# Optimization experiments

Hardware: AMD Instinct MI355X
Metric: run time of the kernel (lower is better)

Reference implementation:

```python
import jax, jax.numpy as jnp
import numpy as np

B, S, D = 4, 4096, 256


def setup_inputs() -> dict:
    key = jax.random.key(0)
    ks = jax.random.split(key, 8)
    inv = 1.0 / np.sqrt(D)
    return {
        "input_tensor": jax.random.normal(ks[0], (B, S, D), dtype=jnp.float32),
        "attention_mask": jax.random.randint(ks[1], (B, S, S), 0, 2) == 1,
        "Wq": jax.random.uniform(ks[2], (D, D), jnp.float32, -inv, inv),
        "bq": jax.random.uniform(ks[3], (D,), jnp.float32, -inv, inv),
        "Wk": jax.random.uniform(ks[4], (D, D), jnp.float32, -inv, inv),
        "bk": jax.random.uniform(ks[5], (D,), jnp.float32, -inv, inv),
        "Wv": jax.random.uniform(ks[6], (D, D), jnp.float32, -inv, inv),
        "bv": jax.random.uniform(ks[7], (D,), jnp.float32, -inv, inv),
    }


def reference(input_tensor, attention_mask, Wq, bq, Wk, bk, Wv, bv):
    # Linear projections: y = x @ W.T + b  (nn.Linear convention, W is [out,in])
    query = jnp.einsum("bsd,ed->bse", input_tensor, Wq) + bq
    key = jnp.einsum("bsd,ed->bse", input_tensor, Wk) + bk
    value = jnp.einsum("bsd,ed->bse", input_tensor, Wv) + bv
    # Faithful quirk: original scales by sqrt(query.size(1)) == sqrt(seq_len)
    scale = jnp.asarray(query.shape[1], query.dtype) ** 0.5
    scores = jnp.einsum("bqd,bkd->bqk", query, key) / scale  # [B,S,S]
    scores = jnp.where(attention_mask, jnp.asarray(-1e9, scores.dtype), scores)
    attn = jax.nn.softmax(scores, axis=-1)
    # dropout with p=0.0 is identity (eval-mode reference)
    context = jnp.einsum("bqk,bkd->bqd", attn, value)
    return context
```

## Files before the change

### kernel.cpp

```cpp
#include <hip/hip_runtime.h>
#include <hip/hip_bf16.h>
#include <stdint.h>

#define BB 4
#define SS 4096
#define DD 256

typedef __attribute__((ext_vector_type(4))) float f32x4;
typedef __attribute__((ext_vector_type(8))) short s16x8;

__device__ __forceinline__ ushort f2bf(float f) {
  __hip_bfloat16 h = __float2bfloat16(f);
  return __builtin_bit_cast(ushort, h);
}

__global__ void convert_kernel(const float* __restrict__ X,
                               const float* __restrict__ Wq,
                               const float* __restrict__ Wk,
                               const float* __restrict__ Wv,
                               const float* __restrict__ bq,
                               const float* __restrict__ bk,
                               const float* __restrict__ bv,
                               ushort* __restrict__ Xb,
                               ushort* __restrict__ Wb,
                               float* __restrict__ bias) {
  int tid = blockIdx.x * blockDim.x + threadIdx.x;
  int stride = gridDim.x * blockDim.x;
  const int NX4 = (BB * SS * DD) / 4;
  for (int i = tid; i < NX4; i += stride) {
    float4 v = ((const float4*)X)[i];
    ushort4 o = { f2bf(v.x), f2bf(v.y), f2bf(v.z), f2bf(v.w) };
    ((ushort4*)Xb)[i] = o;
  }
  const int NW4 = (DD * DD) / 4;
  for (int i = tid; i < NW4; i += stride) {
    float4 a = ((const float4*)Wq)[i];
    float4 b = ((const float4*)Wk)[i];
    float4 c = ((const float4*)Wv)[i];
    ushort4 oa = { f2bf(a.x), f2bf(a.y), f2bf(a.z), f2bf(a.w) };
    ushort4 ob = { f2bf(b.x), f2bf(b.y), f2bf(b.z), f2bf(b.w) };
    ushort4 oc = { f2bf(c.x), f2bf(c.y), f2bf(c.z), f2bf(c.w) };
    ((ushort4*)Wb)[i]           = oa;
    ((ushort4*)Wb)[NW4 + i]     = ob;
    ((ushort4*)Wb)[2 * NW4 + i] = oc;
  }
  if (tid < DD) {
    bias[tid]          = bq[tid];
    bias[DD + tid]     = bk[tid];
    bias[2 * DD + tid] = bv[tid];
  }
}

#define LROW 40

__global__ __launch_bounds__(256) void proj_gemm(const ushort* __restrict__ Xb,
                                                 const ushort* __restrict__ Wb,
                                                 const float* __restrict__ bias,
                                                 ushort* __restrict__ Qb,
                                                 ushort* __restrict__ Kb,
                                                 ushort* __restrict__ Vt) {
  __shared__ ushort Al[128 * LROW];
  __shared__ ushort Bl[128 * LROW];
  const int m0 = blockIdx.x * 128;
  const int n0 = blockIdx.y * 128;
  const int t = threadIdx.x;
  const int lane = t & 63;
  const int w = t >> 6;
  const int wr = w & 1, wc = w >> 1;
  const int col = lane & 15;
  const int quad = lane >> 4;

  f32x4 acc[4][4];
#pragma unroll
  for (int i = 0; i < 4; i++)
#pragma unroll
    for (int j = 0; j < 4; j++) acc[i][j] = f32x4{0.f, 0.f, 0.f, 0.f};

  const int ci0 = t, ci1 = 256 + t;
  const int r0 = ci0 >> 2, c0 = ci0 & 3;
  const int r1 = ci1 >> 2, c1 = ci1 & 3;

  s16x8 pa0 = *(const s16x8*)(Xb + (m0 + r0) * DD + c0 * 8);
  s16x8 pa1 = *(const s16x8*)(Xb + (m0 + r1) * DD + c1 * 8);
  s16x8 pb0 = *(const s16x8*)(Wb + (n0 + r0) * DD + c0 * 8);
  s16x8 pb1 = *(const s16x8*)(Wb + (n0 + r1) * DD + c1 * 8);

  for (int kk = 0; kk < DD; kk += 32) {
    __syncthreads();
    *(s16x8*)&Al[r0 * LROW + c0 * 8] = pa0;
    *(s16x8*)&Al[r1 * LROW + c1 * 8] = pa1;
    *(s16x8*)&Bl[r0 * LROW + c0 * 8] = pb0;
    *(s16x8*)&Bl[r1 * LROW + c1 * 8] = pb1;
    __syncthreads();
    const int kn = kk + 32;
    if (kn < DD) {
      pa0 = *(const s16x8*)(Xb + (m0 + r0) * DD + kn + c0 * 8);
      pa1 = *(const s16x8*)(Xb + (m0 + r1) * DD + kn + c1 * 8);
      pb0 = *(const s16x8*)(Wb + (n0 + r0) * DD + kn + c0 * 8);
      pb1 = *(const s16x8*)(Wb + (n0 + r1) * DD + kn + c1 * 8);
    }
    s16x8 af[4], bfr[4];
#pragma unroll
    for (int mi = 0; mi < 4; mi++)
      af[mi] = *(const s16x8*)&Al[(wr * 64 + mi * 16 + col) * LROW + quad * 8];
#pragma unroll
    for (int ni = 0; ni < 4; ni++)
      bfr[ni] = *(const s16x8*)&Bl[(wc * 64 + ni * 16 + col) * LROW + quad * 8];
#pragma unroll
    for (int mi = 0; mi < 4; mi++)
#pragma unroll
      for (int ni = 0; ni < 4; ni++)
        acc[mi][ni] = __builtin_amdgcn_mfma_f32_16x16x32_bf16(af[mi], bfr[ni], acc[mi][ni], 0, 0, 0);
  }

  const int region = n0 >> 8;
#pragma unroll
  for (int mi = 0; mi < 4; mi++) {
    const int gm = m0 + wr * 64 + mi * 16 + quad * 4;
#pragma unroll
    for (int ni = 0; ni < 4; ni++) {
      const int gn = n0 + wc * 64 + ni * 16 + col;
      const float bb = bias[gn];
      f32x4 v = acc[mi][ni];
      if (region == 0) {
#pragma unroll
        for (int rg = 0; rg < 4; rg++)
          Qb[(gm + rg) * DD + gn] = f2bf((v[rg] + bb) * 0.015625f);
      } else if (region == 1) {
        const int d = gn - 256;
#pragma unroll
        for (int rg = 0; rg < 4; rg++)
          Kb[(gm + rg) * DD + d] = f2bf(v[rg] + bb);
      } else {
        const int d = gn - 512;
        const int b = gm >> 12;
        const int s = gm & (SS - 1);
        ushort4 o = { f2bf(v[0] + bb), f2bf(v[1] + bb), f2bf(v[2] + bb), f2bf(v[3] + bb) };
        *(ushort4*)&Vt[((size_t)(b << 8) + d) * SS + s] = o;
      }
    }
  }
}

#define NKT 32
#define KROW 264
#define VROW 40
#define PROW 40

__global__ __launch_bounds__(256) void attn_kernel(const ushort* __restrict__ Qb,
                                                   const ushort* __restrict__ Kb,
                                                   const ushort* __restrict__ Vt,
                                                   const int* __restrict__ mask,
                                                   float* __restrict__ out) {
  __shared__ ushort Kl[NKT * KROW];
  __shared__ ushort Vl[DD * VROW];
  __shared__ ushort Pl[4][16 * PROW];

  const int qt = blockIdx.x;
  const int b = blockIdx.y;
  const int t = threadIdx.x;
  const int lane = t & 63;
  const int w = t >> 6;
  const int col = lane & 15;
  const int quad = lane >> 4;

  const int q0 = qt * 64;
  const int qrow = q0 + w * 16;

  s16x8 qf[8];
  {
    const ushort* qp = Qb + ((size_t)b * SS + qrow + col) * DD + quad * 8;
#pragma unroll
    for (int dc = 0; dc < 8; dc++) qf[dc] = *(const s16x8*)(qp + dc * 32);
  }

  int kr[4], kc[4], vd[4], vc[4];
#pragma unroll
  for (int i = 0; i < 4; i++) {
    const int ci = i * 256 + t;
    kr[i] = ci >> 5; kc[i] = ci & 31;
    vd[i] = ci >> 2; vc[i] = ci & 3;
  }

  const ushort* Kg = Kb + (size_t)b * SS * DD;
  const ushort* Vg = Vt + (size_t)b * DD * SS;
  const int* Mg = mask + ((size_t)b * SS + q0 + w * 16 + quad * 4) * SS;

  f32x4 Oc[16];
#pragma unroll
  for (int i = 0; i < 16; i++) Oc[i] = f32x4{0.f, 0.f, 0.f, 0.f};
  float m_i[4] = {-INFINITY, -INFINITY, -INFINITY, -INFINITY};
  float l_i[4] = {0.f, 0.f, 0.f, 0.f};

  s16x8 pk[4], pv[4];
  int pm[2][4];
#pragma unroll
  for (int i = 0; i < 4; i++) {
    pk[i] = *(const s16x8*)(Kg + (size_t)kr[i] * DD + kc[i] * 8);
    pv[i] = *(const s16x8*)(Vg + (size_t)vd[i] * SS + vc[i] * 8);
  }
#pragma unroll
  for (int jt = 0; jt < 2; jt++)
#pragma unroll
    for (int rg = 0; rg < 4; rg++) pm[jt][rg] = Mg[rg * SS + jt * 16 + col];

  const int NT = SS / NKT;
  for (int tt = 0; tt < NT; tt++) {
    __syncthreads();
#pragma unroll
    for (int i = 0; i < 4; i++) {
      *(s16x8*)&Kl[kr[i] * KROW + kc[i] * 8] = pk[i];
      *(s16x8*)&Vl[vd[i] * VROW + vc[i] * 8] = pv[i];
    }
    __syncthreads();
    int mcur[2][4];
#pragma unroll
    for (int jt = 0; jt < 2; jt++)
#pragma unroll
      for (int rg = 0; rg < 4; rg++) mcur[jt][rg] = pm[jt][rg];
    if (tt + 1 < NT) {
      const int k0n = (tt + 1) * NKT;
#pragma unroll
      for (int i = 0; i < 4; i++) {
        pk[i] = *(const s16x8*)(Kg + ((size_t)k0n + kr[i]) * DD + kc[i] * 8);
        pv[i] = *(const s16x8*)(Vg + (size_t)vd[i] * SS + k0n + vc[i] * 8);
      }
#pragma unroll
      for (int jt = 0; jt < 2; jt++)
#pragma unroll
        for (int rg = 0; rg < 4; rg++) pm[jt][rg] = Mg[rg * SS + k0n + jt * 16 + col];
    }

    f32x4 st[2];
#pragma unroll
    for (int jt = 0; jt < 2; jt++) {
      f32x4 s = f32x4{0.f, 0.f, 0.f, 0.f};
#pragma unroll
      for (int dc = 0; dc < 8; dc++) {
        s16x8 kb = *(const s16x8*)&Kl[(jt * 16 + col) * KROW + dc * 32 + quad * 8];
        s = __builtin_amdgcn_mfma_f32_16x16x32_bf16(qf[dc], kb, s, 0, 0, 0);
      }
      st[jt] = s;
    }
#pragma unroll
    for (int jt = 0; jt < 2; jt++)
#pragma unroll
      for (int rg = 0; rg < 4; rg++)
        if (mcur[jt][rg]) st[jt][rg] = -1e9f;

    float al[4];
#pragma unroll
    for (int rg = 0; rg < 4; rg++) {
      float v = fmaxf(st[0][rg], st[1][rg]);
      v = fmaxf(v, __shfl_xor(v, 1));
      v = fmaxf(v, __shfl_xor(v, 2));
      v = fmaxf(v, __shfl_xor(v, 4));
      v = fmaxf(v, __shfl_xor(v, 8));
      const float mn = fmaxf(m_i[rg], v);
      al[rg] = __expf(m_i[rg] - mn);
      m_i[rg] = mn;
    }
#pragma unroll
    for (int rg = 0; rg < 4; rg++) {
      const float p0 = __expf(st[0][rg] - m_i[rg]);
      const float p1 = __expf(st[1][rg] - m_i[rg]);
      st[0][rg] = p0; st[1][rg] = p1;
      float s2 = p0 + p1;
      s2 += __shfl_xor(s2, 1);
      s2 += __shfl_xor(s2, 2);
      s2 += __shfl_xor(s2, 4);
      s2 += __shfl_xor(s2, 8);
      l_i[rg] = l_i[rg] * al[rg] + s2;
    }
#pragma unroll
    for (int dt = 0; dt < 16; dt++)
#pragma unroll
      for (int rg = 0; rg < 4; rg++) Oc[dt][rg] *= al[rg];

#pragma unroll
    for (int jt = 0; jt < 2; jt++)
#pragma unroll
      for (int rg = 0; rg < 4; rg++)
        Pl[w][(quad * 4 + rg) * PROW + jt * 16 + col] = f2bf(st[jt][rg]);
    s16x8 pa = *(const s16x8*)&Pl[w][col * PROW + quad * 8];

#pragma unroll
    for (int dt = 0; dt < 16; dt++) {
      s16x8 vb = *(const s16x8*)&Vl[(dt * 16 + col) * VROW + quad * 8];
      Oc[dt] = __builtin_amdgcn_mfma_f32_16x16x32_bf16(pa, vb, Oc[dt], 0, 0, 0);
    }
  }

  float inv[4];
#pragma unroll
  for (int rg = 0; rg < 4; rg++) inv[rg] = 1.0f / l_i[rg];
  float* op = out + ((size_t)b * SS + qrow + quad * 4) * DD;
#pragma unroll
  for (int dt = 0; dt < 16; dt++)
#pragma unroll
    for (int rg = 0; rg < 4; rg++)
      op[rg * DD + dt * 16 + col] = Oc[dt][rg] * inv[rg];
}

extern "C" void kernel_launch(void* const* d_in, const int* in_sizes, int n_in,
                              void* d_out, int out_size, void* d_ws, size_t ws_size,
                              hipStream_t stream) {
  const float* X  = (const float*)d_in[0];
  const int* mask = (const int*)d_in[1];
  const float* Wq = (const float*)d_in[2];
  const float* bq = (const float*)d_in[3];
  const float* Wk = (const float*)d_in[4];
  const float* bk = (const float*)d_in[5];
  const float* Wv = (const float*)d_in[6];
  const float* bv = (const float*)d_in[7];
  float* out = (float*)d_out;

  ushort* base = (ushort*)d_ws;
  ushort* Xb = base;
  ushort* Wb = Xb + (size_t)BB * SS * DD;
  ushort* Qb = Wb + (size_t)3 * DD * DD;
  ushort* Kb = Qb + (size_t)BB * SS * DD;
  ushort* Vt = Kb + (size_t)BB * SS * DD;
  float* bias = (float*)(Vt + (size_t)BB * SS * DD);

  convert_kernel<<<1024, 256, 0, stream>>>(X, Wq, Wk, Wv, bq, bk, bv, Xb, Wb, bias);
  proj_gemm<<<dim3(128, 6), 256, 0, stream>>>(Xb, Wb, bias, Qb, Kb, Vt);
  attn_kernel<<<dim3(64, 4), 256, 0, stream>>>(Qb, Kb, Vt, mask, out);
}
```

Baseline: 619.4 us.

## Split attention over key dimension and merge partial softmax results

Partitions the key sequence into four chunks handled by separate blocks along a new grid dimension. Each block writes unnormalized partial outputs plus running max and sum, and a new merge kernel combines them with log-sum-exp rescaling. This is meant to raise the number of concurrent blocks from one per CU, to hide memory latency on mask and K/V loads. It adds extra global traffic for the partial outputs and one more kernel launch, and reuses the staging workspace for the partials.

```diff
diff --git a/kernel.cpp b/kernel.cpp
--- a/kernel.cpp
+++ b/kernel.cpp
@@ -5,6 +5,8 @@
 #define BB 4
 #define SS 4096
 #define DD 256
+#define KSPLIT 4
+#define KCHUNK (SS / KSPLIT)
 
 typedef __attribute__((ext_vector_type(4))) float f32x4;
 typedef __attribute__((ext_vector_type(8))) short s16x8;
@@ -151,13 +153,17 @@
                                                    const ushort* __restrict__ Kb,
                                                    const ushort* __restrict__ Vt,
                                                    const int* __restrict__ mask,
-                                                   float* __restrict__ out) {
+                                                   float* __restrict__ Opart,
+                                                   float* __restrict__ Mst,
+                                                   float* __restrict__ Lst) {
   __shared__ ushort Kl[NKT * KROW];
   __shared__ ushort Vl[DD * VROW];
   __shared__ ushort Pl[4][16 * PROW];
 
   const int qt = blockIdx.x;
   const int b = blockIdx.y;
+  const int kz = blockIdx.z;
+  const int kbase = kz * KCHUNK;
   const int t = threadIdx.x;
   const int lane = t & 63;
   const int w = t >> 6;
@@ -182,9 +188,9 @@
     vd[i] = ci >> 2; vc[i] = ci & 3;
   }
 
-  const ushort* Kg = Kb + (size_t)b * SS * DD;
-  const ushort* Vg = Vt + (size_t)b * DD * SS;
-  const int* Mg = mask + ((size_t)b * SS + q0 + w * 16 + quad * 4) * SS;
+  const ushort* Kg = Kb + (size_t)b * SS * DD + (size_t)kbase * DD;
+  const ushort* Vg = Vt + (size_t)b * DD * SS + kbase;
+  const int* Mg = mask + ((size_t)b * SS + q0 + w * 16 + quad * 4) * SS + kbase;
 
   f32x4 Oc[16];
 #pragma unroll
@@ -204,7 +210,7 @@
 #pragma unroll
     for (int rg = 0; rg < 4; rg++) pm[jt][rg] = Mg[rg * SS + jt * 16 + col];
 
-  const int NT = SS / NKT;
+  const int NT = KCHUNK / NKT;
   for (int tt = 0; tt < NT; tt++) {
     __syncthreads();
 #pragma unroll
@@ -291,15 +297,45 @@
     }
   }
 
-  float inv[4];
-#pragma unroll
-  for (int rg = 0; rg < 4; rg++) inv[rg] = 1.0f / l_i[rg];
-  float* op = out + ((size_t)b * SS + qrow + quad * 4) * DD;
+  float* op = Opart + (((size_t)kz * BB + b) * SS + qrow + quad * 4) * DD;
 #pragma unroll
   for (int dt = 0; dt < 16; dt++)
 #pragma unroll
     for (int rg = 0; rg < 4; rg++)
-      op[rg * DD + dt * 16 + col] = Oc[dt][rg] * inv[rg];
+      op[rg * DD + dt * 16 + col] = Oc[dt][rg];
+  if (col == 0) {
+    const size_t si = ((size_t)kz * BB + b) * SS + qrow + quad * 4;
+#pragma unroll
+    for (int rg = 0; rg < 4; rg++) {
+      Mst[si + rg] = m_i[rg];
+      Lst[si + rg] = l_i[rg];
+    }
+  }
+}
+
+__global__ __launch_bounds__(256) void merge_kernel(const float* __restrict__ Opart,
+                                                    const float* __restrict__ Mst,
+                                                    const float* __restrict__ Lst,
+                                                    float* __restrict__ out) {
+  const int row = blockIdx.x;
+  const int d = threadIdx.x;
+  const int NR = BB * SS;
+  float m[KSPLIT], l[KSPLIT];
+  float M = -INFINITY;
+#pragma unroll
+  for (int z = 0; z < KSPLIT; z++) {
+    m[z] = Mst[(size_t)z * NR + row];
+    l[z] = Lst[(size_t)z * NR + row];
+    M = fmaxf(M, m[z]);
+  }
+  float wsum = 0.f, acc = 0.f;
+#pragma unroll
+  for (int z = 0; z < KSPLIT; z++) {
+    const float wz = __expf(m[z] - M);
+    wsum += wz * l[z];
+    acc += wz * Opart[((size_t)z * NR + row) * DD + d];
+  }
+  out[(size_t)row * DD + d] = acc / wsum;
 }
 
 extern "C" void kernel_launch(void* const* d_in, const int* in_sizes, int n_in,
@@ -315,15 +351,19 @@
   const float* bv = (const float*)d_in[7];
   float* out = (float*)d_out;
 
-  ushort* base = (ushort*)d_ws;
-  ushort* Xb = base;
-  ushort* Wb = Xb + (size_t)BB * SS * DD;
-  ushort* Qb = Wb + (size_t)3 * DD * DD;
-  ushort* Kb = Qb + (size_t)BB * SS * DD;
-  ushort* Vt = Kb + (size_t)BB * SS * DD;
-  float* bias = (float*)(Vt + (size_t)BB * SS * DD);
+  char* base = (char*)d_ws;
+  ushort* Qb = (ushort*)(base);
+  ushort* Kb = (ushort*)(base + 8388608);
+  ushort* Vt = (ushort*)(base + 16777216);
+  float* bias = (float*)(base + 25165824);
+  float* Mst = (float*)(base + 25169920);
+  float* Lst = (float*)(base + 25432064);
+  float* Opart = (float*)(base + 25694208);
+  ushort* Xb = (ushort*)(base + 25694208);
+  ushort* Wb = (ushort*)(base + 25694208 + 8388608);
 
   convert_kernel<<<1024, 256, 0, stream>>>(X, Wq, Wk, Wv, bq, bk, bv, Xb, Wb, bias);
   proj_gemm<<<dim3(128, 6), 256, 0, stream>>>(Xb, Wb, bias, Qb, Kb, Vt);
-  attn_kernel<<<dim3(64, 4), 256, 0, stream>>>(Qb, Kb, Vt, mask, out);
-}
+  attn_kernel<<<dim3(64, BB, KSPLIT), 256, 0, stream>>>(Qb, Kb, Vt, mask, Opart, Mst, Lst);
+  merge_kernel<<<BB * SS, 256, 0, stream>>>(Opart, Mst, Lst, out);
+}
```

Result: slower. 639.8 us (+3.3%).
